# Performance work log

Measured on AMD Instinct MI355X. Metric: run time of the kernel, lower is better.

Reference implementation:

```python
import jax, jax.numpy as jnp
import numpy as np

B, S, H, D, R = 2, 2048, 16, 128, 16
HID = H * D
ROPE_BASE = 10000.0


def _rotate_half(x):
    x1, x2 = x[..., : D // 2], x[..., D // 2:]
    return jnp.concatenate((-x2, x1), axis=-1)


def _sin_cos(position_ids):
    # full-dim RoPE (rope_fraction == 1)
    inv_freq = 1.0 / (ROPE_BASE ** (jnp.arange(0, D, 2, dtype=jnp.float32) / D))  # [D/2]
    freqs = position_ids.astype(jnp.float32)[..., None] * inv_freq  # [B,S,D/2]
    emb = jnp.concatenate((freqs, freqs), axis=-1)  # [B,S,D]
    # add head axis -> [B,1,S,D]
    return jnp.sin(emb)[:, None], jnp.cos(emb)[:, None]


def setup_inputs() -> dict:
    key = jax.random.key(0)
    ks = jax.random.split(key, 6)
    q = jax.random.normal(ks[0], (B, S, HID), dtype=jnp.float32)
    k = jax.random.normal(ks[1], (B, S, HID), dtype=jnp.float32)
    v = jax.random.normal(ks[2], (B, S, HID), dtype=jnp.float32)
    position_ids = jnp.tile(jnp.arange(S, dtype=jnp.int64)[None], (B, 1))
    causal = jnp.tril(jnp.ones((S, S), dtype=bool))
    attention_mask = jnp.where(causal, 0.0, -1e9).astype(jnp.float32)
    attention_mask = jnp.broadcast_to(attention_mask[None, None], (B, 1, S, S))
    k_registers = jax.random.normal(ks[3], (1, H, R, D), dtype=jnp.float32)
    v_registers = jax.random.normal(ks[4], (1, H, R, D), dtype=jnp.float32)
    return {
        "query_states": q,
        "key_states": k,
        "value_states": v,
        "position_ids": position_ids,
        "attention_mask": attention_mask,
        "k_registers": k_registers,
        "v_registers": v_registers,
    }


def reference(query_states, key_states, value_states, position_ids,
              attention_mask, k_registers, v_registers):
    bsz, q_len, _ = query_states.shape
    # [B,S,H*D] -> [B,H,S,D]
    q = query_states.reshape(bsz, q_len, H, D).transpose(0, 2, 1, 3)
    k = key_states.reshape(bsz, -1, H, D).transpose(0, 2, 1, 3)
    v = value_states.reshape(bsz, -1, H, D).transpose(0, 2, 1, 3)

    sin, cos = _sin_cos(position_ids)
    q = q * cos + _rotate_half(q) * sin
    k = k * cos + _rotate_half(k) * sin

    # concat learned register K/V tokens along kv-length
    k = jnp.concatenate((k, jnp.broadcast_to(k_registers, (bsz, H, R, D))), axis=2)
    v = jnp.concatenate((v, jnp.broadcast_to(v_registers, (bsz, H, R, D))), axis=2)
    mask = jnp.concatenate(
        (attention_mask,
         jnp.zeros(attention_mask.shape[:-1] + (R,), dtype=attention_mask.dtype)),
        axis=-1)

    scale = 1.0 / np.sqrt(D).astype(np.float32)
    scores = jnp.einsum('bhqd,bhkd->bhqk', q, k * scale) + mask  # [B,H,S,S+R]
    probs = jax.nn.softmax(scores.astype(jnp.float32), axis=-1).astype(q.dtype)
    out = jnp.einsum('bhqk,bhkd->bhqd', probs, v)
    return out.transpose(0, 2, 1, 3).reshape(bsz, q_len, H * D)
```

## Files before the change

kernel.cpp:

```cpp
#include <hip/hip_runtime.h>

#define S_LEN 2048
#define HID   2048
#define NH    16
#define HD    128
#define NREG  16
#define KPAD  2112
#define NBH   32

typedef float f32x16 __attribute__((ext_vector_type(16)));
typedef short s16x8  __attribute__((ext_vector_type(8)));

#define ROPE_C  0.20762050593046014f
#define INV2PI  0.15915494309189535f
#define TWOPI   6.283185307179586f
#define QSCALE  0.08838834764831845f

__device__ __forceinline__ unsigned short f2bf(float f) {
    union { float f; unsigned int u; } x; x.f = f;
    return (unsigned short)((x.u + 0x7FFFu + ((x.u >> 16) & 1u)) >> 16);
}
__device__ __forceinline__ unsigned short f2bf_t(float f) {
    union { float f; unsigned int u; } x; x.f = f;
    return (unsigned short)(x.u >> 16);
}
__device__ __forceinline__ void gl_lds16(const unsigned short* g, unsigned short* l) {
    __builtin_amdgcn_global_load_lds((const __attribute__((address_space(1))) void*)g,
                                     (__attribute__((address_space(3))) void*)l, 16, 0, 0);
}

__global__ void prep_kernel(const float* __restrict__ k, const float* __restrict__ v,
                            const int* __restrict__ pos,
                            const float* __restrict__ kreg, const float* __restrict__ vreg,
                            unsigned short* __restrict__ Kb, unsigned short* __restrict__ Vt) {
    int kt = blockIdx.x % 33;
    int bh = blockIdx.x / 33;
    int b = bh >> 4, h = bh & 15;
    int tid = threadIdx.x;

    {
        int dh = tid & 63, wv = tid >> 6;
        if (kt < 32) {
            float inv = exp2f((float)dh * -ROPE_C);
            #pragma unroll 4
            for (int j = 0; j < 16; ++j) {
                int key = wv * 16 + j;
                int s = kt * 64 + key;
                float p = (float)pos[b * S_LEN + s];
                float rev = p * inv * INV2PI;
                rev -= rintf(rev);
                float a2 = rev * TWOPI;
                float sn = __sinf(a2), cs = __cosf(a2);
                const float* kp = k + (size_t)(b * S_LEN + s) * HID + h * HD + dh;
                float k1 = kp[0], k2 = kp[64];
                size_t ko = (size_t)(bh * KPAD + s) * HD + dh;
                Kb[ko]      = f2bf(k1 * cs - k2 * sn);
                Kb[ko + 64] = f2bf(k2 * cs + k1 * sn);
            }
        } else {
            #pragma unroll 4
            for (int j = 0; j < 16; ++j) {
                int r = wv * 16 + j;
                float k1 = 0.f, k2 = 0.f;
                if (r < NREG) {
                    const float* kp = kreg + (h * NREG + r) * HD + dh;
                    k1 = kp[0]; k2 = kp[64];
                }
                size_t ko = (size_t)(bh * KPAD + 2048 + r) * HD + dh;
                Kb[ko]      = f2bf(k1);
                Kb[ko + 64] = f2bf(k2);
            }
        }
    }

    __shared__ unsigned short T[64][136];
    {
        int key = tid >> 2, c = tid & 3;
        #pragma unroll
        for (int i = 0; i < 4; ++i) {
            int d0 = c * 32 + i * 8;
            float vals[8];
            if (kt < 32) {
                const float* src = v + (size_t)(b * S_LEN + kt * 64 + key) * HID + h * HD + d0;
                float4 a = *(const float4*)src, bb = *(const float4*)(src + 4);
                vals[0]=a.x; vals[1]=a.y; vals[2]=a.z; vals[3]=a.w;
                vals[4]=bb.x; vals[5]=bb.y; vals[6]=bb.z; vals[7]=bb.w;
            } else if (key < NREG) {
                const float* src = vreg + (h * NREG + key) * HD + d0;
                float4 a = *(const float4*)src, bb = *(const float4*)(src + 4);
                vals[0]=a.x; vals[1]=a.y; vals[2]=a.z; vals[3]=a.w;
                vals[4]=bb.x; vals[5]=bb.y; vals[6]=bb.z; vals[7]=bb.w;
            } else {
                #pragma unroll
                for (int n = 0; n < 8; ++n) vals[n] = 0.f;
            }
            unsigned short tmp[8];
            #pragma unroll
            for (int n = 0; n < 8; ++n) tmp[n] = f2bf(vals[n]);
            *(uint4*)(&T[key][d0]) = *(const uint4*)tmp;
        }
    }
    __syncthreads();
    {
        int d = tid >> 1, half = tid & 1;
        unsigned short buf[32];
        #pragma unroll
        for (int i = 0; i < 32; ++i) buf[i] = T[half * 32 + i][d];
        uint4* dst = (uint4*)(Vt + ((size_t)(bh * HD + d)) * KPAD + kt * 64 + half * 32);
        const uint4* bp = (const uint4*)buf;
        #pragma unroll
        for (int i = 0; i < 4; ++i) dst[i] = bp[i];
    }
}

__global__ __launch_bounds__(256, 2)
void attn_kernel(const float* __restrict__ q, const int* __restrict__ pos,
                 const unsigned short* __restrict__ Kb, const unsigned short* __restrict__ Vt,
                 float* __restrict__ out) {
    __shared__ unsigned short Klds[64 * 128];
    __shared__ unsigned short Vtl[128 * 64];
    __shared__ unsigned short Plds[4 * 32 * 72];

    int idx = blockIdx.x;
    int bh  = idx & 31;
    int j5  = idx >> 5;
    int t   = (idx < 256) ? (15 - 2 * j5) : (2 * (j5 - 8));
    int b = bh >> 4, h = bh & 15;
    int tid = threadIdx.x, w = tid >> 6, lane = tid & 63;
    int l31 = lane & 31, h5 = lane >> 5, l7 = lane & 7;
    int s0q = t * 128;

    const unsigned short* kg[4]; unsigned short* klp[4];
    const unsigned short* vg[4]; unsigned short* vlp[4];
    {
        #pragma unroll
        for (int j = 0; j < 4; ++j) {
            int key = 16 * w + 4 * j + (lane >> 4);
            int gd  = (lane & 15) ^ (key & 7);
            kg[j]  = Kb + ((size_t)bh * KPAD + key) * HD + (gd << 3);
            klp[j] = Klds + (16 * w + 4 * j) * HD;
        }
        #pragma unroll
        for (int j = 0; j < 4; ++j) {
            int d  = 32 * w + 8 * j + (lane >> 3);
            int gk = (lane & 7) ^ (d & 7);
            vg[j]  = Vt + ((size_t)bh * HD + d) * KPAD + (gk << 3);
            vlp[j] = Vtl + (32 * w + 8 * j) * 64;
        }
    }

    s16x8 qa[8];
    {
        int m_loc = w * 32 + l31;
        int s = s0q + m_loc;
        float pp = (float)pos[b * S_LEN + s];
        const float* qrow = q + (size_t)(b * S_LEN + s) * HID + h * HD + h5 * 8;
        float qv[8][8];
        #pragma unroll
        for (int kc = 0; kc < 8; ++kc) {
            float4 a = *(const float4*)(qrow + kc * 16);
            float4 c = *(const float4*)(qrow + kc * 16 + 4);
            qv[kc][0]=a.x; qv[kc][1]=a.y; qv[kc][2]=a.z; qv[kc][3]=a.w;
            qv[kc][4]=c.x; qv[kc][5]=c.y; qv[kc][6]=c.z; qv[kc][7]=c.w;
        }
        #pragma unroll
        for (int kc = 0; kc < 4; ++kc)
            #pragma unroll
            for (int j = 0; j < 8; ++j) {
                int dh = kc * 16 + h5 * 8 + j;
                float inv = exp2f((float)dh * -ROPE_C);
                float rev = pp * inv * INV2PI;
                rev -= rintf(rev);
                float a2 = rev * TWOPI;
                float sn = __sinf(a2), cs = __cosf(a2);
                float qlo = qv[kc][j], qhi = qv[kc + 4][j];
                qa[kc][j]     = (short)f2bf((qlo * cs - qhi * sn) * QSCALE);
                qa[kc + 4][j] = (short)f2bf((qhi * cs + qlo * sn) * QSCALE);
            }
    }

    s16x8 ones_f;
    {
        short o = (l31 == 0) ? (short)0x3F80 : (short)0;
        #pragma unroll
        for (int j = 0; j < 8; ++j) ones_f[j] = o;
    }

    int swz[8];
    #pragma unroll
    for (int kc = 0; kc < 8; ++kc) swz[kc] = (((2 * kc + h5) ^ l7) << 3);

    f32x16 oacc[4], lacc;
    #pragma unroll
    for (int nd = 0; nd < 4; ++nd)
        #pragma unroll
        for (int r = 0; r < 16; ++r) oacc[nd][r] = 0.f;
    #pragma unroll
    for (int r = 0; r < 16; ++r) lacc[r] = 0.f;

    auto stage = [&](int kbase) {
        size_t ko = (size_t)kbase * HD;
        #pragma unroll
        for (int j = 0; j < 4; ++j) gl_lds16(kg[j] + ko, klp[j]);
        #pragma unroll
        for (int j = 0; j < 4; ++j) gl_lds16(vg[j] + kbase, vlp[j]);
    };

    const unsigned short* kfb = Klds + (l31 << 7);
    unsigned short* pwb = Plds + w * (32 * 72);
    unsigned short* pwl = pwb + (4 * h5) * 72 + l31;
    const unsigned short* prl = pwb + l31 * 72 + h5 * 8;

    auto tile = [&](int coff, int mode) {
        int nct = (mode == 2) ? 1 : 2;
        #pragma unroll
        for (int nc = 0; nc < 2; ++nc) {
            if (nc >= nct) break;
            f32x16 sc;
            #pragma unroll
            for (int r = 0; r < 16; ++r) sc[r] = 0.f;
            #pragma unroll
            for (int kc = 0; kc < 8; ++kc) {
                const s16x8 bf = *(const s16x8*)(kfb + nc * (32 * 128) + swz[kc]);
                sc = __builtin_amdgcn_mfma_f32_32x32x16_bf16(qa[kc], bf, sc, 0, 0, 0);
            }
            #pragma unroll
            for (int reg = 0; reg < 16; ++reg) {
                float e = __expf(sc[reg]);
                if (mode == 1) {
                    int rl = (reg & 3) + 8 * (reg >> 2) + 4 * h5;
                    bool valid = (coff + nc * 32 + l31) <= (w * 32 + rl);
                    e = valid ? e : 0.f;
                } else if (mode == 2) {
                    e = (l31 < NREG) ? e : 0.f;
                }
                pwl[((reg & 3) + 8 * (reg >> 2)) * 72 + nc * 32] = f2bf_t(e);
            }
        }
        int kct = (mode == 2) ? 1 : 4;
        #pragma unroll
        for (int kc = 0; kc < 4; ++kc) {
            if (kc >= kct) break;
            const s16x8 pf = *(const s16x8*)(prl + kc * 16);
            lacc = __builtin_amdgcn_mfma_f32_32x32x16_bf16(pf, ones_f, lacc, 0, 0, 0);
            #pragma unroll
            for (int nd = 0; nd < 4; ++nd) {
                const s16x8 vf = *(const s16x8*)(Vtl + ((nd * 32 + l31) << 6) + swz[kc]);
                oacc[nd] = __builtin_amdgcn_mfma_f32_32x32x16_bf16(pf, vf, oacc[nd], 0, 0, 0);
            }
        }
    };

    int nfull = 2 * t;
    for (int kt = 0; kt < nfull; ++kt) {
        __syncthreads();
        stage(kt * 64);
        __syncthreads();
        tile(0, 0);
    }
    #pragma unroll
    for (int dt = 0; dt < 2; ++dt) {
        __syncthreads();
        stage((2 * t + dt) * 64);
        __syncthreads();
        tile(64 * dt, 1);
    }
    __syncthreads();
    stage(2048);
    __syncthreads();
    tile(0, 2);

    #pragma unroll
    for (int reg = 0; reg < 16; ++reg) {
        float lv = __shfl(lacc[reg], lane & 32);
        float invl = 1.0f / lv;
        int rl = (reg & 3) + 8 * (reg >> 2) + 4 * h5;
        size_t row = (size_t)(b * S_LEN + s0q + w * 32 + rl) * HID + h * HD + l31;
        #pragma unroll
        for (int nd = 0; nd < 4; ++nd)
            out[row + nd * 32] = oacc[nd][reg] * invl;
    }
}

extern "C" void kernel_launch(void* const* d_in, const int* in_sizes, int n_in,
                              void* d_out, int out_size, void* d_ws, size_t ws_size,
                              hipStream_t stream) {
    const float* q    = (const float*)d_in[0];
    const float* k    = (const float*)d_in[1];
    const float* v    = (const float*)d_in[2];
    const int*   pos  = (const int*)d_in[3];
    const float* kreg = (const float*)d_in[5];
    const float* vreg = (const float*)d_in[6];
    float* out = (float*)d_out;

    unsigned short* Kb = (unsigned short*)d_ws;
    unsigned short* Vt = Kb + (size_t)NBH * KPAD * HD;

    prep_kernel<<<dim3(NBH * 33), dim3(256), 0, stream>>>(k, v, pos, kreg, vreg, Kb, Vt);
    attn_kernel<<<dim3(512), dim3(256), 0, stream>>>(q, pos, Kb, Vt, out);
}
```

Before: 228.0 us.

## Switch attention MFMAs from 32x32x16 to 16x16x32 tiles with VALU row sums

Rewrites the attention inner loop to use 16x16x32 bf16 MFMAs with two 16-row M tiles per wave, and changes the LDS swizzles for K and V to match the new fragment layout. The softmax denominator is now summed in registers and reduced with cross-lane shuffles at the end, replacing the extra MFMA against a ones vector. This removes one MFMA per k-chunk and changes register use and LDS access patterns. In exchange it adds more VALU work for the sums and more, smaller MFMA instructions.

```diff
diff --git a/kernel.cpp b/kernel.cpp
--- a/kernel.cpp
+++ b/kernel.cpp
@@ -8,8 +8,8 @@
 #define KPAD  2112
 #define NBH   32
 
-typedef float f32x16 __attribute__((ext_vector_type(16)));
-typedef short s16x8  __attribute__((ext_vector_type(8)));
+typedef float f32x4 __attribute__((ext_vector_type(4)));
+typedef short s16x8 __attribute__((ext_vector_type(8)));
 
 #define ROPE_C  0.20762050593046014f
 #define INV2PI  0.15915494309189535f
@@ -127,76 +127,71 @@
     int t   = (idx < 256) ? (15 - 2 * j5) : (2 * (j5 - 8));
     int b = bh >> 4, h = bh & 15;
     int tid = threadIdx.x, w = tid >> 6, lane = tid & 63;
-    int l31 = lane & 31, h5 = lane >> 5, l7 = lane & 7;
+    int quad = lane >> 4, k15 = lane & 15;
     int s0q = t * 128;
 
     const unsigned short* kg[4]; unsigned short* klp[4];
     const unsigned short* vg[4]; unsigned short* vlp[4];
     {
+        int krow = 16 * w + (lane >> 4);
         #pragma unroll
         for (int j = 0; j < 4; ++j) {
-            int key = 16 * w + 4 * j + (lane >> 4);
-            int gd  = (lane & 15) ^ (key & 7);
-            kg[j]  = Kb + ((size_t)bh * KPAD + key) * HD + (gd << 3);
+            int key = krow + 4 * j;
+            kg[j]  = Kb + ((size_t)bh * KPAD + key) * HD + (((lane & 15) ^ (key & 15)) << 3);
             klp[j] = Klds + (16 * w + 4 * j) * HD;
         }
+        int drow = 32 * w + (lane >> 3);
+        int vsw  = ((lane & 7) ^ (lane >> 3)) << 3;
         #pragma unroll
         for (int j = 0; j < 4; ++j) {
-            int d  = 32 * w + 8 * j + (lane >> 3);
-            int gk = (lane & 7) ^ (d & 7);
-            vg[j]  = Vt + ((size_t)bh * HD + d) * KPAD + (gk << 3);
+            vg[j]  = Vt + ((size_t)bh * HD + drow + 8 * j) * KPAD + vsw;
             vlp[j] = Vtl + (32 * w + 8 * j) * 64;
         }
     }
 
-    s16x8 qa[8];
-    {
-        int m_loc = w * 32 + l31;
-        int s = s0q + m_loc;
+    s16x8 qa[2][4];
+    #pragma unroll
+    for (int mt = 0; mt < 2; ++mt) {
+        int s = s0q + w * 32 + mt * 16 + k15;
         float pp = (float)pos[b * S_LEN + s];
-        const float* qrow = q + (size_t)(b * S_LEN + s) * HID + h * HD + h5 * 8;
-        float qv[8][8];
-        #pragma unroll
-        for (int kc = 0; kc < 8; ++kc) {
-            float4 a = *(const float4*)(qrow + kc * 16);
-            float4 c = *(const float4*)(qrow + kc * 16 + 4);
-            qv[kc][0]=a.x; qv[kc][1]=a.y; qv[kc][2]=a.z; qv[kc][3]=a.w;
-            qv[kc][4]=c.x; qv[kc][5]=c.y; qv[kc][6]=c.z; qv[kc][7]=c.w;
-        }
-        #pragma unroll
-        for (int kc = 0; kc < 4; ++kc)
+        const float* qrow = q + (size_t)(b * S_LEN + s) * HID + h * HD + quad * 8;
+        float lo[2][8], hi[2][8];
+        #pragma unroll
+        for (int kc = 0; kc < 2; ++kc) {
+            float4 a  = *(const float4*)(qrow + kc * 32);
+            float4 c  = *(const float4*)(qrow + kc * 32 + 4);
+            lo[kc][0]=a.x; lo[kc][1]=a.y; lo[kc][2]=a.z; lo[kc][3]=a.w;
+            lo[kc][4]=c.x; lo[kc][5]=c.y; lo[kc][6]=c.z; lo[kc][7]=c.w;
+            float4 a2 = *(const float4*)(qrow + kc * 32 + 64);
+            float4 c2 = *(const float4*)(qrow + kc * 32 + 68);
+            hi[kc][0]=a2.x; hi[kc][1]=a2.y; hi[kc][2]=a2.z; hi[kc][3]=a2.w;
+            hi[kc][4]=c2.x; hi[kc][5]=c2.y; hi[kc][6]=c2.z; hi[kc][7]=c2.w;
+        }
+        #pragma unroll
+        for (int kc = 0; kc < 2; ++kc)
             #pragma unroll
             for (int j = 0; j < 8; ++j) {
-                int dh = kc * 16 + h5 * 8 + j;
+                int dh = kc * 32 + quad * 8 + j;
                 float inv = exp2f((float)dh * -ROPE_C);
                 float rev = pp * inv * INV2PI;
                 rev -= rintf(rev);
-                float a2 = rev * TWOPI;
-                float sn = __sinf(a2), cs = __cosf(a2);
-                float qlo = qv[kc][j], qhi = qv[kc + 4][j];
-                qa[kc][j]     = (short)f2bf((qlo * cs - qhi * sn) * QSCALE);
-                qa[kc + 4][j] = (short)f2bf((qhi * cs + qlo * sn) * QSCALE);
-            }
-    }
-
-    s16x8 ones_f;
-    {
-        short o = (l31 == 0) ? (short)0x3F80 : (short)0;
-        #pragma unroll
-        for (int j = 0; j < 8; ++j) ones_f[j] = o;
-    }
-
-    int swz[8];
+                float a2r = rev * TWOPI;
+                float sn = __sinf(a2r), cs = __cosf(a2r);
+                float qlo = lo[kc][j], qhi = hi[kc][j];
+                qa[mt][kc][j]     = (short)f2bf((qlo * cs - qhi * sn) * QSCALE);
+                qa[mt][kc + 2][j] = (short)f2bf((qhi * cs + qlo * sn) * QSCALE);
+            }
+    }
+
+    f32x4 oacc[2][8];
+    float lsum[2][4];
     #pragma unroll
-    for (int kc = 0; kc < 8; ++kc) swz[kc] = (((2 * kc + h5) ^ l7) << 3);
-
-    f32x16 oacc[4], lacc;
-    #pragma unroll
-    for (int nd = 0; nd < 4; ++nd)
-        #pragma unroll
-        for (int r = 0; r < 16; ++r) oacc[nd][r] = 0.f;
-    #pragma unroll
-    for (int r = 0; r < 16; ++r) lacc[r] = 0.f;
+    for (int mt = 0; mt < 2; ++mt) {
+        #pragma unroll
+        for (int nc = 0; nc < 8; ++nc) oacc[mt][nc] = (f32x4){0.f, 0.f, 0.f, 0.f};
+        #pragma unroll
+        for (int r = 0; r < 4; ++r) lsum[mt][r] = 0.f;
+    }
 
     auto stage = [&](int kbase) {
         size_t ko = (size_t)kbase * HD;
@@ -206,47 +201,60 @@
         for (int j = 0; j < 4; ++j) gl_lds16(vg[j] + kbase, vlp[j]);
     };
 
-    const unsigned short* kfb = Klds + (l31 << 7);
-    unsigned short* pwb = Plds + w * (32 * 72);
-    unsigned short* pwl = pwb + (4 * h5) * 72 + l31;
-    const unsigned short* prl = pwb + l31 * 72 + h5 * 8;
-
     auto tile = [&](int coff, int mode) {
-        int nct = (mode == 2) ? 1 : 2;
-        #pragma unroll
-        for (int nc = 0; nc < 2; ++nc) {
-            if (nc >= nct) break;
-            f32x16 sc;
-            #pragma unroll
-            for (int r = 0; r < 16; ++r) sc[r] = 0.f;
-            #pragma unroll
-            for (int kc = 0; kc < 8; ++kc) {
-                const s16x8 bf = *(const s16x8*)(kfb + nc * (32 * 128) + swz[kc]);
-                sc = __builtin_amdgcn_mfma_f32_32x32x16_bf16(qa[kc], bf, sc, 0, 0, 0);
-            }
-            #pragma unroll
-            for (int reg = 0; reg < 16; ++reg) {
-                float e = __expf(sc[reg]);
-                if (mode == 1) {
-                    int rl = (reg & 3) + 8 * (reg >> 2) + 4 * h5;
-                    bool valid = (coff + nc * 32 + l31) <= (w * 32 + rl);
-                    e = valid ? e : 0.f;
-                } else if (mode == 2) {
-                    e = (l31 < NREG) ? e : 0.f;
+        f32x4 sc[2][4];
+        #pragma unroll
+        for (int mt = 0; mt < 2; ++mt)
+            #pragma unroll
+            for (int nc = 0; nc < 4; ++nc) sc[mt][nc] = (f32x4){0.f, 0.f, 0.f, 0.f};
+        #pragma unroll
+        for (int kc = 0; kc < 4; ++kc)
+            #pragma unroll
+            for (int nc = 0; nc < 4; ++nc) {
+                if (mode == 2 && nc > 0) continue;
+                const s16x8 bf = *(const s16x8*)(Klds + (nc * 16 + k15) * HD +
+                                                 (((4 * kc + quad) ^ k15) << 3));
+                #pragma unroll
+                for (int mt = 0; mt < 2; ++mt)
+                    sc[mt][nc] = __builtin_amdgcn_mfma_f32_16x16x32_bf16(qa[mt][kc], bf, sc[mt][nc], 0, 0, 0);
+            }
+        #pragma unroll
+        for (int mt = 0; mt < 2; ++mt) {
+            int rowb = w * 32 + mt * 16 + quad * 4;
+            #pragma unroll
+            for (int r = 0; r < 4; ++r) {
+                float p[4];
+                #pragma unroll
+                for (int nc = 0; nc < 4; ++nc) {
+                    if (mode == 2 && nc > 0) { p[nc] = 0.f; continue; }
+                    float e = __expf(sc[mt][nc][r]);
+                    bool valid = (mode == 1) ? (coff + nc * 16 + k15 <= rowb + r)
+                               : (mode == 2) ? (k15 < NREG) : true;
+                    p[nc] = valid ? e : 0.f;
                 }
-                pwl[((reg & 3) + 8 * (reg >> 2)) * 72 + nc * 32] = f2bf_t(e);
-            }
-        }
-        int kct = (mode == 2) ? 1 : 4;
-        #pragma unroll
-        for (int kc = 0; kc < 4; ++kc) {
-            if (kc >= kct) break;
-            const s16x8 pf = *(const s16x8*)(prl + kc * 16);
-            lacc = __builtin_amdgcn_mfma_f32_32x32x16_bf16(pf, ones_f, lacc, 0, 0, 0);
-            #pragma unroll
-            for (int nd = 0; nd < 4; ++nd) {
-                const s16x8 vf = *(const s16x8*)(Vtl + ((nd * 32 + l31) << 6) + swz[kc]);
-                oacc[nd] = __builtin_amdgcn_mfma_f32_32x32x16_bf16(pf, vf, oacc[nd], 0, 0, 0);
+                lsum[mt][r] += (p[0] + p[1]) + (p[2] + p[3]);
+                int prow = w * (32 * 72) + (mt * 16 + quad * 4 + r) * 72 + k15;
+                Plds[prow]      = f2bf_t(p[0]);
+                Plds[prow + 16] = f2bf_t(p[1]);
+                Plds[prow + 32] = f2bf_t(p[2]);
+                Plds[prow + 48] = f2bf_t(p[3]);
+            }
+        }
+        #pragma unroll
+        for (int kc = 0; kc < 2; ++kc) {
+            if (mode == 2 && kc > 0) break;
+            s16x8 pf[2];
+            #pragma unroll
+            for (int mt = 0; mt < 2; ++mt)
+                pf[mt] = *(const s16x8*)(Plds + w * (32 * 72) + (mt * 16 + k15) * 72 +
+                                         kc * 32 + quad * 8);
+            #pragma unroll
+            for (int nc = 0; nc < 8; ++nc) {
+                const s16x8 vf = *(const s16x8*)(Vtl + (nc * 16 + k15) * 64 +
+                                                 (((4 * kc + quad) ^ (k15 & 7)) << 3));
+                #pragma unroll
+                for (int mt = 0; mt < 2; ++mt)
+                    oacc[mt][nc] = __builtin_amdgcn_mfma_f32_16x16x32_bf16(pf[mt], vf, oacc[mt][nc], 0, 0, 0);
             }
         }
     };
@@ -271,15 +279,19 @@
     tile(0, 2);
 
     #pragma unroll
-    for (int reg = 0; reg < 16; ++reg) {
-        float lv = __shfl(lacc[reg], lane & 32);
-        float invl = 1.0f / lv;
-        int rl = (reg & 3) + 8 * (reg >> 2) + 4 * h5;
-        size_t row = (size_t)(b * S_LEN + s0q + w * 32 + rl) * HID + h * HD + l31;
-        #pragma unroll
-        for (int nd = 0; nd < 4; ++nd)
-            out[row + nd * 32] = oacc[nd][reg] * invl;
-    }
+    for (int mt = 0; mt < 2; ++mt)
+        #pragma unroll
+        for (int r = 0; r < 4; ++r) {
+            float lv = lsum[mt][r];
+            #pragma unroll
+            for (int off = 1; off < 16; off <<= 1) lv += __shfl_xor(lv, off);
+            float invl = 1.0f / lv;
+            size_t row = (size_t)(b * S_LEN + s0q + w * 32 + mt * 16 + quad * 4 + r) * HID
+                         + h * HD + k15;
+            #pragma unroll
+            for (int nc = 0; nc < 8; ++nc)
+                out[row + nc * 16] = oacc[mt][nc][r] * invl;
+        }
 }
 
 extern "C" void kernel_launch(void* const* d_in, const int* in_sizes, int n_in,
```

After: 226.9 us. Within noise of the previous version (-0.5%).
